# Performance work log

Measured on AMD Instinct MI355X. Metric: run time of the kernel, lower is better.

The kernel has to match this reference:

```python
import jax, jax.numpy as jnp
import numpy as np

HEADS = 8
HEAD_DIM = 32
DIM = 256
INNER = HEADS * HEAD_DIM  # 256


def setup_inputs() -> dict:
    key = jax.random.key(0)
    ks = jax.random.split(key, 6)
    b, h, w, c = 16, 64, 64, DIM
    x = jax.random.normal(ks[0], (b, h, w, c), dtype=jnp.float32)
    # Flax Dense kernels: (in_features, out_features); q/k/v have no bias.
    wq = jax.random.normal(ks[1], (c, INNER), dtype=jnp.float32) / np.sqrt(c)
    wk = jax.random.normal(ks[2], (c, INNER), dtype=jnp.float32) / np.sqrt(c)
    wv = jax.random.normal(ks[3], (c, INNER), dtype=jnp.float32) / np.sqrt(c)
    wo = jax.random.normal(ks[4], (INNER, DIM), dtype=jnp.float32) / np.sqrt(INNER)
    bo = jnp.zeros((DIM,), dtype=jnp.float32)
    return {"x": x, "wq": wq, "wk": wk, "wv": wv, "wo": wo, "bo": bo}


def _split_heads(t, b, h, w):
    # 'b h w (n d) -> b n h w d'
    return t.reshape(b, h, w, HEADS, HEAD_DIM).transpose(0, 3, 1, 2, 4)


def reference(x, wq, wk, wv, wo, bo):
    b, h, w, c = x.shape
    scale = HEAD_DIM ** (-0.5)
    q = _split_heads(x @ wq, b, h, w)  # [b, n, h, w, d]
    k = _split_heads(x @ wk, b, h, w)
    v = _split_heads(x @ wv, b, h, w)
    # attention along width axis per (batch, head, height-row)
    attn = jnp.einsum('bnhqd,bnhkd->bnhqk', q, k) * scale  # [b,n,h,w,w]
    attn = jax.nn.softmax(attn, axis=-1)
    out = jnp.einsum('bnhqk,bnhkd->bnhqd', attn, v)  # [b,n,h,w,d]
    # 'b n h w d -> b h w (n d)'
    out = out.transpose(0, 2, 3, 1, 4).reshape(b, h, w, INNER)
    return out @ wo + bo
```

## Files before the change

kernel.cpp:

```cpp
#include <hip/hip_runtime.h>
#include <hip/hip_bf16.h>

typedef short bf16x8 __attribute__((ext_vector_type(8)));
typedef float f32x4  __attribute__((ext_vector_type(4)));

__device__ __forceinline__ unsigned short f2bf(float f) {
    union { __hip_bfloat16 b; unsigned short u; } v;
    v.b = __hip_bfloat16(f);
    return v.u;
}

__device__ __forceinline__ f32x4 mfma_bf16(bf16x8 a, bf16x8 b, f32x4 c) {
    return __builtin_amdgcn_mfma_f32_16x16x32_bf16(a, b, c, 0, 0, 0);
}

__device__ __forceinline__ bf16x8 pack2(f32x4 lo, f32x4 hi) {
    bf16x8 r;
    r[0] = (short)f2bf(lo[0]); r[1] = (short)f2bf(lo[1]);
    r[2] = (short)f2bf(lo[2]); r[3] = (short)f2bf(lo[3]);
    r[4] = (short)f2bf(hi[0]); r[5] = (short)f2bf(hi[1]);
    r[6] = (short)f2bf(hi[2]); r[7] = (short)f2bf(hi[3]);
    return r;
}

__global__ __launch_bounds__(256) void prep_weights(
    const float* __restrict__ wq, const float* __restrict__ wk,
    const float* __restrict__ wv, const float* __restrict__ wo,
    unsigned short* __restrict__ wt)
{
    const int s = blockIdx.x * 256 + threadIdx.x;
    const int mat  = s >> 13;
    const int h    = (s >> 10) & 7;
    const int t    = (s >> 9) & 1;
    const int kk   = (s >> 6) & 7;
    const int lane = s & 63;
    const int l15  = lane & 15;
    const int g    = lane >> 4;
    const float* src = (mat == 0) ? wq : (mat == 1) ? wk : (mat == 2) ? wv : wo;
    const int n  = h * 32 + t * 16 + l15;
    const int k0 = kk * 32 + g * 8;
    unsigned short* dst = wt + (size_t)s * 8;
#pragma unroll
    for (int j = 0; j < 8; ++j)
        dst[j] = f2bf(src[(k0 + j) * 256 + n]);
}

#define XS_STRIDE 264

__global__ __launch_bounds__(512, 2) void win_attn(
    const float* __restrict__ x,
    const unsigned short* __restrict__ wt,
    const float* __restrict__ bo,
    float* __restrict__ out)
{
    __shared__ unsigned short lds[33792];
    unsigned short* Xs = lds;
    unsigned short* Os = lds + 16896;

    const int tid  = threadIdx.x;
    const int wid  = tid >> 6;
    const int lane = tid & 63;
    const int l15  = lane & 15;
    const int g    = lane >> 4;

    const bf16x8* WF = reinterpret_cast<const bf16x8*>(wt);
    const int wbase = (wid * 2) * 8 * 64 + lane;
#define WFRAG(mat, t, kk) WF[(mat) * 8192 + wbase + ((t) * 8 + (kk)) * 64]

    const long long base_tok = (long long)blockIdx.x * 64;
    const float* xblk = x + base_tok * 256;

    const f32x4 fz = {0.f, 0.f, 0.f, 0.f};

#pragma unroll
    for (int i = 0; i < 8; ++i) {
        int p   = tid + i * 512;
        int tok = p >> 6;
        int col = (p & 63) * 4;
        float4 v = reinterpret_cast<const float4*>(xblk)[p];
        ushort4 h;
        h.x = f2bf(v.x); h.y = f2bf(v.y); h.z = f2bf(v.z); h.w = f2bf(v.w);
        *reinterpret_cast<ushort4*>(&Xs[tok * XS_STRIDE + col]) = h;
    }
    __syncthreads();

    bf16x8 qtf[4], ktf[4], vtf[2][2];
    {
        f32x4 qt[2][4] = {{fz, fz, fz, fz}, {fz, fz, fz, fz}};
        f32x4 kt[2][4] = {{fz, fz, fz, fz}, {fz, fz, fz, fz}};
        f32x4 vac[4][2] = {{fz, fz}, {fz, fz}, {fz, fz}, {fz, fz}};
#pragma unroll
        for (int kk = 0; kk < 8; ++kk) {
            bf16x8 bx[4];
#pragma unroll
            for (int nt = 0; nt < 4; ++nt)
                bx[nt] = *reinterpret_cast<const bf16x8*>(&Xs[(nt * 16 + l15) * XS_STRIDE + kk * 32 + g * 8]);
            bf16x8 awq[2], awk[2], bv[2];
#pragma unroll
            for (int t = 0; t < 2; ++t) {
                awq[t] = WFRAG(0, t, kk);
                awk[t] = WFRAG(1, t, kk);
                bv[t]  = WFRAG(2, t, kk);
            }
#pragma unroll
            for (int mt = 0; mt < 2; ++mt)
#pragma unroll
                for (int nt = 0; nt < 4; ++nt) {
                    qt[mt][nt] = mfma_bf16(awq[mt], bx[nt], qt[mt][nt]);
                    kt[mt][nt] = mfma_bf16(awk[mt], bx[nt], kt[mt][nt]);
                }
#pragma unroll
            for (int mi = 0; mi < 4; ++mi)
#pragma unroll
                for (int dh = 0; dh < 2; ++dh)
                    vac[mi][dh] = mfma_bf16(bx[mi], bv[dh], vac[mi][dh]);
        }
#pragma unroll
        for (int nt = 0; nt < 4; ++nt) {
            qtf[nt] = pack2(qt[0][nt], qt[1][nt]);
            ktf[nt] = pack2(kt[0][nt], kt[1][nt]);
        }
#pragma unroll
        for (int dh = 0; dh < 2; ++dh) {
            vtf[0][dh] = pack2(vac[0][dh], vac[1][dh]);
            vtf[1][dh] = pack2(vac[2][dh], vac[3][dh]);
        }
    }

    constexpr float kC = 0.25501817419392105f;
#pragma unroll
    for (int ni = 0; ni < 4; ++ni) {
        f32x4 st[4];
#pragma unroll
        for (int mi = 0; mi < 4; ++mi)
            st[mi] = mfma_bf16(ktf[mi], qtf[ni], fz);
        float m = st[0][0];
#pragma unroll
        for (int mi = 0; mi < 4; ++mi)
#pragma unroll
            for (int r = 0; r < 4; ++r) m = fmaxf(m, st[mi][r]);
        m = fmaxf(m, __shfl_xor(m, 16));
        m = fmaxf(m, __shfl_xor(m, 32));
        float sum = 0.f;
#pragma unroll
        for (int mi = 0; mi < 4; ++mi)
#pragma unroll
            for (int r = 0; r < 4; ++r) {
                st[mi][r] = exp2f((st[mi][r] - m) * kC);
                sum += st[mi][r];
            }
        sum += __shfl_xor(sum, 16);
        sum += __shfl_xor(sum, 32);
        float inv = 1.0f / sum;
        bf16x8 pa[2];
#pragma unroll
        for (int kk = 0; kk < 2; ++kk) {
            bf16x8 t;
#pragma unroll
            for (int j = 0; j < 4; ++j) {
                t[j]     = (short)f2bf(st[2 * kk][j] * inv);
                t[4 + j] = (short)f2bf(st[2 * kk + 1][j] * inv);
            }
            pa[kk] = t;
        }
        f32x4 oacc[2] = {fz, fz};
#pragma unroll
        for (int kk = 0; kk < 2; ++kk)
#pragma unroll
            for (int dh = 0; dh < 2; ++dh)
                oacc[dh] = mfma_bf16(pa[kk], vtf[kk][dh], oacc[dh]);
#pragma unroll
        for (int dh = 0; dh < 2; ++dh)
#pragma unroll
            for (int r = 0; r < 4; ++r)
                Os[(ni * 16 + g * 4 + r) * XS_STRIDE + wid * 32 + dh * 16 + l15] = f2bf(oacc[dh][r]);
    }
    __syncthreads();

    {
        f32x4 yacc[4][2] = {{fz, fz}, {fz, fz}, {fz, fz}, {fz, fz}};
#pragma unroll
        for (int kk = 0; kk < 8; ++kk) {
            bf16x8 a[4], b[2];
#pragma unroll
            for (int ni = 0; ni < 2; ++ni)
                b[ni] = WFRAG(3, ni, kk);
#pragma unroll
            for (int mi = 0; mi < 4; ++mi)
                a[mi] = *reinterpret_cast<const bf16x8*>(&Os[(mi * 16 + l15) * XS_STRIDE + kk * 32 + g * 8]);
#pragma unroll
            for (int mi = 0; mi < 4; ++mi)
#pragma unroll
                for (int ni = 0; ni < 2; ++ni)
                    yacc[mi][ni] = mfma_bf16(a[mi], b[ni], yacc[mi][ni]);
        }
#pragma unroll
        for (int mi = 0; mi < 4; ++mi) {
#pragma unroll
            for (int ni = 0; ni < 2; ++ni) {
                int col = wid * 32 + ni * 16 + l15;
                float bv = bo[col];
#pragma unroll
                for (int r = 0; r < 4; ++r) {
                    int row = mi * 16 + g * 4 + r;
                    out[(base_tok + row) * 256 + col] = yacc[mi][ni][r] + bv;
                }
            }
        }
    }
#undef WFRAG
}

extern "C" void kernel_launch(void* const* d_in, const int* in_sizes, int n_in,
                              void* d_out, int out_size, void* d_ws, size_t ws_size,
                              hipStream_t stream) {
    const float* x  = (const float*)d_in[0];
    const float* wq = (const float*)d_in[1];
    const float* wk = (const float*)d_in[2];
    const float* wv = (const float*)d_in[3];
    const float* wo = (const float*)d_in[4];
    const float* bo = (const float*)d_in[5];
    unsigned short* wt = (unsigned short*)d_ws;
    float* out = (float*)d_out;

    prep_weights<<<128, 256, 0, stream>>>(wq, wk, wv, wo, wt);
    win_attn<<<1024, 512, 0, stream>>>(x, wt, bo, out);
}
```

Measured before the change: 78.10 us.

## Split fused QKV projection into sequential V, Q, K passes to cut register pressure

Splits the single fused QKV projection loop into three passes (V first, then Q, then K), each with its own accumulators, and raises the launch-bounds minimum blocks per CU from 2 to 4. The aim is to lower peak live registers so more wavefronts can be resident per CU and latency hides better. In exchange the X tile is read from LDS three times instead of once, and the tighter register budget may cause spills. LDS use per block (about 66 KB) may also cap how many blocks actually fit on a CU.

```diff
diff --git a/kernel.cpp b/kernel.cpp
--- a/kernel.cpp
+++ b/kernel.cpp
@@ -47,7 +47,7 @@
 
 #define XS_STRIDE 264
 
-__global__ __launch_bounds__(512, 2) void win_attn(
+__global__ __launch_bounds__(512, 4) void win_attn(
     const float* __restrict__ x,
     const unsigned short* __restrict__ wt,
     const float* __restrict__ bo,
@@ -84,47 +84,63 @@
     }
     __syncthreads();
 
-    bf16x8 qtf[4], ktf[4], vtf[2][2];
+    bf16x8 vtf[2][2];
+#pragma unroll
+    for (int dh = 0; dh < 2; ++dh) {
+        f32x4 vac[4] = {fz, fz, fz, fz};
+#pragma unroll
+        for (int kk = 0; kk < 8; ++kk) {
+            bf16x8 bv = WFRAG(2, dh, kk);
+#pragma unroll
+            for (int mi = 0; mi < 4; ++mi) {
+                bf16x8 a = *reinterpret_cast<const bf16x8*>(&Xs[(mi * 16 + l15) * XS_STRIDE + kk * 32 + g * 8]);
+                vac[mi] = mfma_bf16(a, bv, vac[mi]);
+            }
+        }
+        vtf[0][dh] = pack2(vac[0], vac[1]);
+        vtf[1][dh] = pack2(vac[2], vac[3]);
+    }
+
+    bf16x8 qtf[4];
     {
         f32x4 qt[2][4] = {{fz, fz, fz, fz}, {fz, fz, fz, fz}};
-        f32x4 kt[2][4] = {{fz, fz, fz, fz}, {fz, fz, fz, fz}};
-        f32x4 vac[4][2] = {{fz, fz}, {fz, fz}, {fz, fz}, {fz, fz}};
-#pragma unroll
-        for (int kk = 0; kk < 8; ++kk) {
-            bf16x8 bx[4];
+#pragma unroll
+        for (int kk = 0; kk < 8; ++kk) {
+            bf16x8 aw[2], bx[4];
+            aw[0] = WFRAG(0, 0, kk);
+            aw[1] = WFRAG(0, 1, kk);
 #pragma unroll
             for (int nt = 0; nt < 4; ++nt)
                 bx[nt] = *reinterpret_cast<const bf16x8*>(&Xs[(nt * 16 + l15) * XS_STRIDE + kk * 32 + g * 8]);
-            bf16x8 awq[2], awk[2], bv[2];
-#pragma unroll
-            for (int t = 0; t < 2; ++t) {
-                awq[t] = WFRAG(0, t, kk);
-                awk[t] = WFRAG(1, t, kk);
-                bv[t]  = WFRAG(2, t, kk);
-            }
 #pragma unroll
             for (int mt = 0; mt < 2; ++mt)
 #pragma unroll
-                for (int nt = 0; nt < 4; ++nt) {
-                    qt[mt][nt] = mfma_bf16(awq[mt], bx[nt], qt[mt][nt]);
-                    kt[mt][nt] = mfma_bf16(awk[mt], bx[nt], kt[mt][nt]);
-                }
-#pragma unroll
-            for (int mi = 0; mi < 4; ++mi)
-#pragma unroll
-                for (int dh = 0; dh < 2; ++dh)
-                    vac[mi][dh] = mfma_bf16(bx[mi], bv[dh], vac[mi][dh]);
-        }
-#pragma unroll
-        for (int nt = 0; nt < 4; ++nt) {
-            qtf[nt] = pack2(qt[0][nt], qt[1][nt]);
-            ktf[nt] = pack2(kt[0][nt], kt[1][nt]);
-        }
-#pragma unroll
-        for (int dh = 0; dh < 2; ++dh) {
-            vtf[0][dh] = pack2(vac[0][dh], vac[1][dh]);
-            vtf[1][dh] = pack2(vac[2][dh], vac[3][dh]);
-        }
+                for (int nt = 0; nt < 4; ++nt)
+                    qt[mt][nt] = mfma_bf16(aw[mt], bx[nt], qt[mt][nt]);
+        }
+#pragma unroll
+        for (int nt = 0; nt < 4; ++nt) qtf[nt] = pack2(qt[0][nt], qt[1][nt]);
+    }
+
+    bf16x8 ktf[4];
+    {
+        f32x4 kt[2][4] = {{fz, fz, fz, fz}, {fz, fz, fz, fz}};
+#pragma unroll
+        for (int kk = 0; kk < 8; ++kk) {
+            bf16x8 aw[2], bx[4];
+            aw[0] = WFRAG(1, 0, kk);
+            aw[1] = WFRAG(1, 1, kk);
+#pragma unroll
+            for (int nt = 0; nt < 4; ++nt)
+                bx[nt] = *reinterpret_cast<const bf16x8*>(&Xs[(nt * 16 + l15) * XS_STRIDE + kk * 32 + g * 8]);
+#pragma unroll
+            for (int mt = 0; mt < 2; ++mt)
+#pragma unroll
+                for (int nt = 0; nt < 4; ++nt)
+                    kt[mt][nt] = mfma_bf16(aw[mt], bx[nt], kt[mt][nt]);
+        }
+#pragma unroll
+        for (int nt = 0; nt < 4; ++nt) ktf[nt] = pack2(kt[0][nt], kt[1][nt]);
     }
 
     constexpr float kC = 0.25501817419392105f;
@@ -182,9 +198,8 @@
 #pragma unroll
         for (int kk = 0; kk < 8; ++kk) {
             bf16x8 a[4], b[2];
-#pragma unroll
-            for (int ni = 0; ni < 2; ++ni)
-                b[ni] = WFRAG(3, ni, kk);
+            b[0] = WFRAG(3, 0, kk);
+            b[1] = WFRAG(3, 1, kk);
 #pragma unroll
             for (int mi = 0; mi < 4; ++mi)
                 a[mi] = *reinterpret_cast<const bf16x8*>(&Os[(mi * 16 + l15) * XS_STRIDE + kk * 32 + g * 8]);
```

After: 158.5 us. +102.9%, slower.

## Persistent blocks with async global-to-LDS prefetch of next x tile

Applied to the files above, without the earlier changes.

The launch changes to 256 persistent blocks that each process four 64-token tiles. While the current tile is computed, the next tile's fp32 x data is prefetched straight into LDS with global_load_lds. MFMA phases are bracketed with s_setprio to favour compute waves. Each block now needs an extra 64KB fp32 LDS staging buffer, which likely cuts occupancy to one block per CU, and the grid is only one block per CU.

```diff
diff --git a/kernel.cpp b/kernel.cpp
--- a/kernel.cpp
+++ b/kernel.cpp
@@ -12,6 +12,12 @@
 
 __device__ __forceinline__ f32x4 mfma_bf16(bf16x8 a, bf16x8 b, f32x4 c) {
     return __builtin_amdgcn_mfma_f32_16x16x32_bf16(a, b, c, 0, 0, 0);
+}
+
+__device__ __forceinline__ void gload_lds16(const float* g, float* l) {
+    __builtin_amdgcn_global_load_lds(
+        (const __attribute__((address_space(1))) unsigned int*)g,
+        (__attribute__((address_space(3))) unsigned int*)l, 16, 0, 0);
 }
 
 __device__ __forceinline__ bf16x8 pack2(f32x4 lo, f32x4 hi) {
@@ -53,9 +59,10 @@
     const float* __restrict__ bo,
     float* __restrict__ out)
 {
-    __shared__ unsigned short lds[33792];
-    unsigned short* Xs = lds;
-    unsigned short* Os = lds + 16896;
+    __shared__ unsigned short lds16[33792];
+    __shared__ float XfF[16384];
+    unsigned short* Xs = lds16;
+    unsigned short* Os = lds16 + 16896;
 
     const int tid  = threadIdx.x;
     const int wid  = tid >> 6;
@@ -67,143 +74,170 @@
     const int wbase = (wid * 2) * 8 * 64 + lane;
 #define WFRAG(mat, t, kk) WF[(mat) * 8192 + wbase + ((t) * 8 + (kk)) * 64]
 
-    const long long base_tok = (long long)blockIdx.x * 64;
-    const float* xblk = x + base_tok * 256;
-
     const f32x4 fz = {0.f, 0.f, 0.f, 0.f};
-
-#pragma unroll
-    for (int i = 0; i < 8; ++i) {
-        int p   = tid + i * 512;
-        int tok = p >> 6;
-        int col = (p & 63) * 4;
-        float4 v = reinterpret_cast<const float4*>(xblk)[p];
-        ushort4 h;
-        h.x = f2bf(v.x); h.y = f2bf(v.y); h.z = f2bf(v.z); h.w = f2bf(v.w);
-        *reinterpret_cast<ushort4*>(&Xs[tok * XS_STRIDE + col]) = h;
+    constexpr float kC = 0.25501817419392105f;
+
+    {
+        const float* src = x + (size_t)blockIdx.x * 16384;
+#pragma unroll
+        for (int i = 0; i < 8; ++i) {
+            int chunk = wid * 8 + i;
+            gload_lds16(src + chunk * 256 + lane * 4, XfF + chunk * 256);
+        }
     }
-    __syncthreads();
-
-    bf16x8 qtf[4], ktf[4], vtf[2][2];
-    {
-        f32x4 qt[2][4] = {{fz, fz, fz, fz}, {fz, fz, fz, fz}};
-        f32x4 kt[2][4] = {{fz, fz, fz, fz}, {fz, fz, fz, fz}};
-        f32x4 vac[4][2] = {{fz, fz}, {fz, fz}, {fz, fz}, {fz, fz}};
-#pragma unroll
-        for (int kk = 0; kk < 8; ++kk) {
-            bf16x8 bx[4];
-#pragma unroll
-            for (int nt = 0; nt < 4; ++nt)
-                bx[nt] = *reinterpret_cast<const bf16x8*>(&Xs[(nt * 16 + l15) * XS_STRIDE + kk * 32 + g * 8]);
-            bf16x8 awq[2], awk[2], bv[2];
-#pragma unroll
-            for (int t = 0; t < 2; ++t) {
-                awq[t] = WFRAG(0, t, kk);
-                awk[t] = WFRAG(1, t, kk);
-                bv[t]  = WFRAG(2, t, kk);
-            }
-#pragma unroll
-            for (int mt = 0; mt < 2; ++mt)
-#pragma unroll
-                for (int nt = 0; nt < 4; ++nt) {
-                    qt[mt][nt] = mfma_bf16(awq[mt], bx[nt], qt[mt][nt]);
-                    kt[mt][nt] = mfma_bf16(awk[mt], bx[nt], kt[mt][nt]);
-                }
+
+    for (int it = 0; it < 4; ++it) {
+        const int bid = it * 256 + (int)blockIdx.x;
+        asm volatile("s_waitcnt vmcnt(0)" ::: "memory");
+        __syncthreads();
+#pragma unroll
+        for (int i = 0; i < 4; ++i) {
+            int p   = tid + i * 512;
+            int tok = p >> 5;
+            int col = (p & 31) * 8;
+            const float4 lo = *reinterpret_cast<const float4*>(&XfF[p * 8]);
+            const float4 hi = *reinterpret_cast<const float4*>(&XfF[p * 8 + 4]);
+            bf16x8 w;
+            w[0] = (short)f2bf(lo.x); w[1] = (short)f2bf(lo.y);
+            w[2] = (short)f2bf(lo.z); w[3] = (short)f2bf(lo.w);
+            w[4] = (short)f2bf(hi.x); w[5] = (short)f2bf(hi.y);
+            w[6] = (short)f2bf(hi.z); w[7] = (short)f2bf(hi.w);
+            *reinterpret_cast<bf16x8*>(&Xs[tok * XS_STRIDE + col]) = w;
+        }
+        __syncthreads();
+        if (it < 3) {
+            const float* src = x + (size_t)(bid + 256) * 16384;
+#pragma unroll
+            for (int i = 0; i < 8; ++i) {
+                int chunk = wid * 8 + i;
+                gload_lds16(src + chunk * 256 + lane * 4, XfF + chunk * 256);
+            }
+        }
+
+        bf16x8 qtf[4], ktf[4], vtf[2][2];
+        {
+            f32x4 qt[2][4] = {{fz, fz, fz, fz}, {fz, fz, fz, fz}};
+            f32x4 kt[2][4] = {{fz, fz, fz, fz}, {fz, fz, fz, fz}};
+            f32x4 vac[4][2] = {{fz, fz}, {fz, fz}, {fz, fz}, {fz, fz}};
+            __builtin_amdgcn_s_setprio(1);
+#pragma unroll
+            for (int kk = 0; kk < 8; ++kk) {
+                bf16x8 bx[4];
+#pragma unroll
+                for (int nt = 0; nt < 4; ++nt)
+                    bx[nt] = *reinterpret_cast<const bf16x8*>(&Xs[(nt * 16 + l15) * XS_STRIDE + kk * 32 + g * 8]);
+                bf16x8 awq[2], awk[2], bv[2];
+#pragma unroll
+                for (int t = 0; t < 2; ++t) {
+                    awq[t] = WFRAG(0, t, kk);
+                    awk[t] = WFRAG(1, t, kk);
+                    bv[t]  = WFRAG(2, t, kk);
+                }
+#pragma unroll
+                for (int mt = 0; mt < 2; ++mt)
+#pragma unroll
+                    for (int nt = 0; nt < 4; ++nt) {
+                        qt[mt][nt] = mfma_bf16(awq[mt], bx[nt], qt[mt][nt]);
+                        kt[mt][nt] = mfma_bf16(awk[mt], bx[nt], kt[mt][nt]);
+                    }
+#pragma unroll
+                for (int mi = 0; mi < 4; ++mi)
+#pragma unroll
+                    for (int dh = 0; dh < 2; ++dh)
+                        vac[mi][dh] = mfma_bf16(bx[mi], bv[dh], vac[mi][dh]);
+            }
+            __builtin_amdgcn_s_setprio(0);
+#pragma unroll
+            for (int nt = 0; nt < 4; ++nt) {
+                qtf[nt] = pack2(qt[0][nt], qt[1][nt]);
+                ktf[nt] = pack2(kt[0][nt], kt[1][nt]);
+            }
+#pragma unroll
+            for (int dh = 0; dh < 2; ++dh) {
+                vtf[0][dh] = pack2(vac[0][dh], vac[1][dh]);
+                vtf[1][dh] = pack2(vac[2][dh], vac[3][dh]);
+            }
+        }
+
+#pragma unroll
+        for (int ni = 0; ni < 4; ++ni) {
+            f32x4 st[4];
 #pragma unroll
             for (int mi = 0; mi < 4; ++mi)
+                st[mi] = mfma_bf16(ktf[mi], qtf[ni], fz);
+            float m = st[0][0];
+#pragma unroll
+            for (int mi = 0; mi < 4; ++mi)
+#pragma unroll
+                for (int r = 0; r < 4; ++r) m = fmaxf(m, st[mi][r]);
+            m = fmaxf(m, __shfl_xor(m, 16));
+            m = fmaxf(m, __shfl_xor(m, 32));
+            float sum = 0.f;
+#pragma unroll
+            for (int mi = 0; mi < 4; ++mi)
+#pragma unroll
+                for (int r = 0; r < 4; ++r) {
+                    st[mi][r] = exp2f((st[mi][r] - m) * kC);
+                    sum += st[mi][r];
+                }
+            sum += __shfl_xor(sum, 16);
+            sum += __shfl_xor(sum, 32);
+            float inv = 1.0f / sum;
+            bf16x8 pa[2];
+#pragma unroll
+            for (int kk = 0; kk < 2; ++kk) {
+                bf16x8 t;
+#pragma unroll
+                for (int j = 0; j < 4; ++j) {
+                    t[j]     = (short)f2bf(st[2 * kk][j] * inv);
+                    t[4 + j] = (short)f2bf(st[2 * kk + 1][j] * inv);
+                }
+                pa[kk] = t;
+            }
+            f32x4 oacc[2] = {fz, fz};
+#pragma unroll
+            for (int kk = 0; kk < 2; ++kk)
 #pragma unroll
                 for (int dh = 0; dh < 2; ++dh)
-                    vac[mi][dh] = mfma_bf16(bx[mi], bv[dh], vac[mi][dh]);
-        }
-#pragma unroll
-        for (int nt = 0; nt < 4; ++nt) {
-            qtf[nt] = pack2(qt[0][nt], qt[1][nt]);
-            ktf[nt] = pack2(kt[0][nt], kt[1][nt]);
-        }
-#pragma unroll
-        for (int dh = 0; dh < 2; ++dh) {
-            vtf[0][dh] = pack2(vac[0][dh], vac[1][dh]);
-            vtf[1][dh] = pack2(vac[2][dh], vac[3][dh]);
-        }
-    }
-
-    constexpr float kC = 0.25501817419392105f;
-#pragma unroll
-    for (int ni = 0; ni < 4; ++ni) {
-        f32x4 st[4];
-#pragma unroll
-        for (int mi = 0; mi < 4; ++mi)
-            st[mi] = mfma_bf16(ktf[mi], qtf[ni], fz);
-        float m = st[0][0];
-#pragma unroll
-        for (int mi = 0; mi < 4; ++mi)
-#pragma unroll
-            for (int r = 0; r < 4; ++r) m = fmaxf(m, st[mi][r]);
-        m = fmaxf(m, __shfl_xor(m, 16));
-        m = fmaxf(m, __shfl_xor(m, 32));
-        float sum = 0.f;
-#pragma unroll
-        for (int mi = 0; mi < 4; ++mi)
-#pragma unroll
-            for (int r = 0; r < 4; ++r) {
-                st[mi][r] = exp2f((st[mi][r] - m) * kC);
-                sum += st[mi][r];
-            }
-        sum += __shfl_xor(sum, 16);
-        sum += __shfl_xor(sum, 32);
-        float inv = 1.0f / sum;
-        bf16x8 pa[2];
-#pragma unroll
-        for (int kk = 0; kk < 2; ++kk) {
-            bf16x8 t;
-#pragma unroll
-            for (int j = 0; j < 4; ++j) {
-                t[j]     = (short)f2bf(st[2 * kk][j] * inv);
-                t[4 + j] = (short)f2bf(st[2 * kk + 1][j] * inv);
-            }
-            pa[kk] = t;
-        }
-        f32x4 oacc[2] = {fz, fz};
-#pragma unroll
-        for (int kk = 0; kk < 2; ++kk)
+                    oacc[dh] = mfma_bf16(pa[kk], vtf[kk][dh], oacc[dh]);
 #pragma unroll
             for (int dh = 0; dh < 2; ++dh)
-                oacc[dh] = mfma_bf16(pa[kk], vtf[kk][dh], oacc[dh]);
-#pragma unroll
-        for (int dh = 0; dh < 2; ++dh)
-#pragma unroll
-            for (int r = 0; r < 4; ++r)
-                Os[(ni * 16 + g * 4 + r) * XS_STRIDE + wid * 32 + dh * 16 + l15] = f2bf(oacc[dh][r]);
-    }
-    __syncthreads();
-
-    {
-        f32x4 yacc[4][2] = {{fz, fz}, {fz, fz}, {fz, fz}, {fz, fz}};
-#pragma unroll
-        for (int kk = 0; kk < 8; ++kk) {
-            bf16x8 a[4], b[2];
-#pragma unroll
-            for (int ni = 0; ni < 2; ++ni)
-                b[ni] = WFRAG(3, ni, kk);
-#pragma unroll
-            for (int mi = 0; mi < 4; ++mi)
-                a[mi] = *reinterpret_cast<const bf16x8*>(&Os[(mi * 16 + l15) * XS_STRIDE + kk * 32 + g * 8]);
-#pragma unroll
-            for (int mi = 0; mi < 4; ++mi)
-#pragma unroll
-                for (int ni = 0; ni < 2; ++ni)
-                    yacc[mi][ni] = mfma_bf16(a[mi], b[ni], yacc[mi][ni]);
-        }
-#pragma unroll
-        for (int mi = 0; mi < 4; ++mi) {
-#pragma unroll
-            for (int ni = 0; ni < 2; ++ni) {
-                int col = wid * 32 + ni * 16 + l15;
-                float bv = bo[col];
-#pragma unroll
-                for (int r = 0; r < 4; ++r) {
-                    int row = mi * 16 + g * 4 + r;
-                    out[(base_tok + row) * 256 + col] = yacc[mi][ni][r] + bv;
+#pragma unroll
+                for (int r = 0; r < 4; ++r)
+                    Os[(ni * 16 + g * 4 + r) * XS_STRIDE + wid * 32 + dh * 16 + l15] = f2bf(oacc[dh][r]);
+        }
+        __syncthreads();
+
+        {
+            f32x4 yacc[4][2] = {{fz, fz}, {fz, fz}, {fz, fz}, {fz, fz}};
+            __builtin_amdgcn_s_setprio(1);
+#pragma unroll
+            for (int kk = 0; kk < 8; ++kk) {
+                bf16x8 a[4], b[2];
+                b[0] = WFRAG(3, 0, kk);
+                b[1] = WFRAG(3, 1, kk);
+#pragma unroll
+                for (int mi = 0; mi < 4; ++mi)
+                    a[mi] = *reinterpret_cast<const bf16x8*>(&Os[(mi * 16 + l15) * XS_STRIDE + kk * 32 + g * 8]);
+#pragma unroll
+                for (int mi = 0; mi < 4; ++mi)
+#pragma unroll
+                    for (int ni = 0; ni < 2; ++ni)
+                        yacc[mi][ni] = mfma_bf16(a[mi], b[ni], yacc[mi][ni]);
+            }
+            __builtin_amdgcn_s_setprio(0);
+            const long long base_tok = (long long)bid * 64;
+#pragma unroll
+            for (int mi = 0; mi < 4; ++mi) {
+#pragma unroll
+                for (int ni = 0; ni < 2; ++ni) {
+                    int col = wid * 32 + ni * 16 + l15;
+                    float bv = bo[col];
+#pragma unroll
+                    for (int r = 0; r < 4; ++r) {
+                        int row = mi * 16 + g * 4 + r;
+                        out[(base_tok + row) * 256 + col] = yacc[mi][ni][r] + bv;
+                    }
                 }
             }
         }
@@ -224,5 +258,5 @@
     float* out = (float*)d_out;
 
     prep_weights<<<128, 256, 0, stream>>>(wq, wk, wv, wo, wt);
-    win_attn<<<1024, 512, 0, stream>>>(x, wt, bo, out);
-}
+    win_attn<<<256, 512, 0, stream>>>(x, wt, bo, out);
+}
```

Measured after the change: 101.1 us. 29.4% more time.
